# Performance work log

Hardware: AMD Instinct MI355X
Metric: run time of the kernel (lower is better)

Reference implementation:

```python
import jax, jax.numpy as jnp
import numpy as np

N = 100000
IN_C = 128
OUT_C = 200
E = 1600000


def gcn_conv(x, edge_index, W, b):
    """PyG GCNConv: symmetric degree-normalized aggregation with self-loops.
    out[v] = sum_{(u,v) in E+selfloops} d_u^-1/2 d_v^-1/2 (x_u @ W) + b
    """
    n = x.shape[0]
    xw = x @ W  # [N, out]
    loop = jnp.arange(n, dtype=edge_index.dtype)
    row = jnp.concatenate([edge_index[0], loop])  # src
    col = jnp.concatenate([edge_index[1], loop])  # dst
    ones = jnp.ones(row.shape[0], dtype=x.dtype)
    deg = jax.ops.segment_sum(ones, col, num_segments=n)  # in-degree incl. self
    dinv = jnp.where(deg > 0, jax.lax.rsqrt(deg), 0.0)
    norm = dinv[row] * dinv[col]  # [E+N]
    msgs = xw[row] * norm[:, None]  # [E+N, out]
    out = jax.ops.segment_sum(msgs, col, num_segments=n)
    return out + b


def setup_inputs() -> dict:
    key = jax.random.key(0)
    k1, k2, k3, k4 = jax.random.split(key, 4)
    x = jax.random.normal(k1, (N, IN_C), dtype=jnp.float32)
    edge_index = jax.random.randint(k2, (2, E), 0, N, dtype=jnp.int64)
    s1 = 1.0 / np.sqrt(IN_C)
    W1 = jax.random.uniform(k3, (IN_C, OUT_C), dtype=jnp.float32, minval=-s1, maxval=s1)
    b1 = jnp.zeros((OUT_C,), dtype=jnp.float32)
    W2 = jax.random.uniform(k4, (IN_C, OUT_C), dtype=jnp.float32, minval=-s1, maxval=s1)
    b2 = jnp.zeros((OUT_C,), dtype=jnp.float32)
    return {"x": x, "edge_index": edge_index, "W1": W1, "b1": b1, "W2": W2, "b2": b2}


def reference(x, edge_index, W1, b1, W2, b2):
    mu = gcn_conv(x, edge_index, W1, b1)
    logstd = gcn_conv(x, edge_index, W2, b2)
    return (mu, logstd)
```

## Files before the change

### kernel.cpp

```cpp
#include <hip/hip_runtime.h>

#define N_NODES 100000
#define IN_C    128
#define OUT_C   200
#define NT_TILES 13
#define KT_TILES 4

#define PSHIFT  8
#define NPB     256
#define NB      391
#define NB_POW2 512
#define BCAP    5120
#define PART_CH 4096
#define SEQ_P   16
#define SEQ_B   20

typedef __bf16 bf16_t;
typedef bf16_t bf16x8 __attribute__((ext_vector_type(8)));
typedef float  f32x4  __attribute__((ext_vector_type(4)));

__device__ __forceinline__ unsigned int bf16_bits(float f) {
    unsigned int u = __builtin_bit_cast(unsigned int, f);
    return (u + 0x7FFFu + ((u >> 16) & 1u)) >> 16;
}
__device__ __forceinline__ float bf16_lo(unsigned int p) {
    return __builtin_bit_cast(float, p << 16);
}
__device__ __forceinline__ float bf16_hi(unsigned int p) {
    return __builtin_bit_cast(float, p & 0xFFFF0000u);
}

__global__ __launch_bounds__(256) void partition_kernel(
        const int* __restrict__ row, const int* __restrict__ col, int E,
        int* __restrict__ gcount, unsigned int* __restrict__ gbuf) {
    __shared__ int hist[NB];
    __shared__ int base[NB];
    __shared__ int lofs[NB];
    __shared__ int pscan[256];
    __shared__ unsigned int stage[PART_CH];
    __shared__ unsigned short sb[PART_CH];
    const int tid = threadIdx.x;
    const int chunk = blockIdx.x * PART_CH;
    int cend = E - chunk; if (cend > PART_CH) cend = PART_CH;

    for (int i = tid; i < NB; i += 256) hist[i] = 0;
    __syncthreads();

    unsigned int   pay[SEQ_P];
    unsigned short eb[SEQ_P];
    unsigned short sq[SEQ_P];
    #pragma unroll
    for (int k = 0; k < SEQ_P; k++) {
        int i = tid + k * 256;
        eb[k] = 0xFFFFu;
        if (i < cend) {
            int c = __builtin_nontemporal_load(col + chunk + i);
            int r = __builtin_nontemporal_load(row + chunk + i);
            int b = (c >> PSHIFT) & (NB_POW2 - 1);
            if (b >= NB) b = NB - 1;
            pay[k] = (unsigned int)((c & (NPB - 1)) | (r << PSHIFT));
            eb[k]  = (unsigned short)b;
            sq[k]  = (unsigned short)atomicAdd(&hist[b], 1);
        }
    }
    __syncthreads();

    for (int i = tid; i < NB; i += 256)
        base[i] = atomicAdd(&gcount[i], hist[i]);

    int v0 = (2 * tid     < NB) ? hist[2 * tid]     : 0;
    int v1 = (2 * tid + 1 < NB) ? hist[2 * tid + 1] : 0;
    int s = v0 + v1;
    pscan[tid] = s;
    __syncthreads();
    for (int off = 1; off < 256; off <<= 1) {
        int u = (tid >= off) ? pscan[tid - off] : 0;
        __syncthreads();
        pscan[tid] += u;
        __syncthreads();
    }
    int ep = pscan[tid] - s;
    if (2 * tid     < NB) lofs[2 * tid]     = ep;
    if (2 * tid + 1 < NB) lofs[2 * tid + 1] = ep + v0;
    __syncthreads();

    #pragma unroll
    for (int k = 0; k < SEQ_P; k++) {
        if (eb[k] != 0xFFFFu) {
            int p = lofs[eb[k]] + sq[k];
            stage[p] = pay[k];
            sb[p] = eb[k];
        }
    }
    __syncthreads();

    for (int i = tid; i < cend; i += 256) {
        int b = sb[i];
        int p = base[b] + (i - lofs[b]);
        if (p < BCAP) gbuf[(size_t)b * BCAP + p] = stage[i];
    }
}

__global__ __launch_bounds__(256) void build_kernel(
        const unsigned int* __restrict__ gbuf, const int* __restrict__ gcount,
        const float* __restrict__ x,
        int* __restrict__ deg, int* __restrict__ offsets, float* __restrict__ dinv,
        int* __restrict__ csr_src, uint2* __restrict__ xs4, int n) {
    __shared__ int cnt[NPB];
    __shared__ int cur[NPB];
    __shared__ int pscan[256];
    __shared__ int gb[512];
    const int b = blockIdx.x;
    const int tid = threadIdx.x;

    int g0 = (2 * tid     < NB) ? gcount[2 * tid]     : 0;
    int g1 = (2 * tid + 1 < NB) ? gcount[2 * tid + 1] : 0;
    if (g0 > BCAP) g0 = BCAP;
    if (g1 > BCAP) g1 = BCAP;
    int gs = g0 + g1;
    pscan[tid] = gs;
    cnt[tid] = 0;
    __syncthreads();
    for (int off = 1; off < 256; off <<= 1) {
        int u = (tid >= off) ? pscan[tid - off] : 0;
        __syncthreads();
        pscan[tid] += u;
        __syncthreads();
    }
    int gep = pscan[tid] - gs;
    gb[2 * tid]     = gep;
    gb[2 * tid + 1] = gep + g0;
    __syncthreads();

    const int cbase = gb[b];
    int total = gcount[b]; if (total > BCAP) total = BCAP;
    const unsigned int* bp = gbuf + (size_t)b * BCAP;

    unsigned int   ee[SEQ_B];
    unsigned short sq[SEQ_B];
    #pragma unroll
    for (int k = 0; k < SEQ_B; k++) {
        int i = tid + k * 256;
        ee[k] = 0xFFFFFFFFu;
        if (i < total) {
            unsigned int e = __builtin_nontemporal_load(bp + i);
            ee[k] = e;
            sq[k] = (unsigned short)atomicAdd(&cnt[e & (NPB - 1)], 1);
        }
    }
    __syncthreads();

    int c = cnt[tid];
    pscan[tid] = c;
    __syncthreads();
    for (int off = 1; off < 256; off <<= 1) {
        int u = (tid >= off) ? pscan[tid - off] : 0;
        __syncthreads();
        pscan[tid] += u;
        __syncthreads();
    }
    int excl = pscan[tid] - c;
    cur[tid] = excl;
    int v = b * NPB + tid;
    if (v < n) {
        deg[v] = c;
        offsets[v] = cbase + excl;
        dinv[v] = rsqrtf((float)(c + 1));
    }
    __syncthreads();

    #pragma unroll
    for (int k = 0; k < SEQ_B; k++) {
        if (ee[k] != 0xFFFFFFFFu) {
            int p = cur[ee[k] & (NPB - 1)] + (int)sq[k];
            csr_src[cbase + p] = (int)(ee[k] >> PSHIFT);
        }
    }

    int wv = tid >> 6, ln = tid & 63;
    int hlf = ln >> 5, hl2 = ln & 31;
    for (int m = 0; m < 64; m += 2) {
        int local = wv * 64 + m + hlf;
        int nv = b * NPB + local;
        if (nv < n) {
            float dv = rsqrtf((float)(cnt[local] + 1));
            f32x4 f = __builtin_nontemporal_load((const f32x4*)x + (size_t)nv * 32 + hl2);
            uint2 o;
            o.x = bf16_bits(f.x * dv) | (bf16_bits(f.y * dv) << 16);
            o.y = bf16_bits(f.z * dv) | (bf16_bits(f.w * dv) << 16);
            xs4[(size_t)nv * 32 + hl2] = o;
        }
    }
}

__global__ __launch_bounds__(256) void gather_kernel(
        const uint2* __restrict__ xs4, const float* __restrict__ dinv,
        const int* __restrict__ offsets, const int* __restrict__ deg,
        const int* __restrict__ csr_src, uint2* __restrict__ agg4, int n) {
    int wave = threadIdx.x >> 6;
    int lane = threadIdx.x & 63;
    int half = lane >> 5;
    int hl   = lane & 31;
    int v = blockIdx.x * 4 + wave;
    if (v >= n) return;
    float dv = dinv[v];
    int start = offsets[v];
    int cnt = deg[v];
    float ax = 0.f, ay = 0.f, az = 0.f, aw = 0.f;

    const int* cp = csr_src + start;
    int i = 0;
    for (; i + 16 <= cnt; i += 16) {
        int u[8];
        #pragma unroll
        for (int j = 0; j < 8; j++) u[j] = __builtin_nontemporal_load(cp + i + 2 * j + half);
        uint2 t[8];
        #pragma unroll
        for (int j = 0; j < 8; j++) t[j] = xs4[(size_t)u[j] * 32 + hl];
        #pragma unroll
        for (int j = 0; j < 8; j++) {
            ax += bf16_lo(t[j].x); ay += bf16_hi(t[j].x);
            az += bf16_lo(t[j].y); aw += bf16_hi(t[j].y);
        }
    }
    if (i + 8 <= cnt) {
        int u[4];
        #pragma unroll
        for (int j = 0; j < 4; j++) u[j] = __builtin_nontemporal_load(cp + i + 2 * j + half);
        uint2 t[4];
        #pragma unroll
        for (int j = 0; j < 4; j++) t[j] = xs4[(size_t)u[j] * 32 + hl];
        #pragma unroll
        for (int j = 0; j < 4; j++) {
            ax += bf16_lo(t[j].x); ay += bf16_hi(t[j].x);
            az += bf16_lo(t[j].y); aw += bf16_hi(t[j].y);
        }
        i += 8;
    }
    if (i + 4 <= cnt) {
        int u[2];
        #pragma unroll
        for (int j = 0; j < 2; j++) u[j] = __builtin_nontemporal_load(cp + i + 2 * j + half);
        uint2 t[2];
        #pragma unroll
        for (int j = 0; j < 2; j++) t[j] = xs4[(size_t)u[j] * 32 + hl];
        #pragma unroll
        for (int j = 0; j < 2; j++) {
            ax += bf16_lo(t[j].x); ay += bf16_hi(t[j].x);
            az += bf16_lo(t[j].y); aw += bf16_hi(t[j].y);
        }
        i += 4;
    }
    if (i + 2 <= cnt) {
        int u = __builtin_nontemporal_load(cp + i + half);
        uint2 t = xs4[(size_t)u * 32 + hl];
        ax += bf16_lo(t.x); ay += bf16_hi(t.x);
        az += bf16_lo(t.y); aw += bf16_hi(t.y);
        i += 2;
    }
    if (i < cnt && half == 0) {
        int u = __builtin_nontemporal_load(cp + i);
        uint2 t = xs4[(size_t)u * 32 + hl];
        ax += bf16_lo(t.x); ay += bf16_hi(t.x);
        az += bf16_lo(t.y); aw += bf16_hi(t.y);
    }
    ax += __shfl_xor(ax, 32, 64);
    ay += __shfl_xor(ay, 32, 64);
    az += __shfl_xor(az, 32, 64);
    aw += __shfl_xor(aw, 32, 64);
    uint2 s = xs4[(size_t)v * 32 + hl];
    ax += bf16_lo(s.x); ay += bf16_hi(s.x);
    az += bf16_lo(s.y); aw += bf16_hi(s.y);
    if (half == 0) {
        uint2 o;
        o.x = bf16_bits(ax * dv) | (bf16_bits(ay * dv) << 16);
        o.y = bf16_bits(az * dv) | (bf16_bits(aw * dv) << 16);
        agg4[(size_t)v * 32 + hl] = o;
    }
}

__global__ void pack_w_kernel(const float* __restrict__ W1, const float* __restrict__ W2,
                              unsigned short* __restrict__ out) {
    int tid = blockIdx.x * blockDim.x + threadIdx.x;
    if (tid >= 2 * KT_TILES * NT_TILES * 64) return;
    int lane = tid & 63;
    int nt = (tid >> 6) % NT_TILES;
    int kt = (tid / (64 * NT_TILES)) % KT_TILES;
    int h  = tid / (64 * NT_TILES * KT_TILES);
    const float* W = h ? W2 : W1;
    int q = lane >> 4, r = lane & 15;
    int nn = nt * 16 + r;
    size_t dst = ((size_t)((nt * 2 + h) * KT_TILES + kt)) * 512 + (size_t)lane * 8;
    for (int j = 0; j < 8; j++) {
        int k = kt * 32 + q * 8 + j;
        float val = (nn < OUT_C) ? W[(size_t)k * OUT_C + nn] : 0.f;
        out[dst + j] = (unsigned short)bf16_bits(val);
    }
}

__global__ __launch_bounds__(256) void gemm_mfma_kernel(
        const unsigned short* __restrict__ agg,
        const unsigned short* __restrict__ Wpk,
        const float* __restrict__ b1, const float* __restrict__ b2,
        float* __restrict__ mu, float* __restrict__ ls, int M) {
    __shared__ uint4 Bs[2][512];
    int tid  = threadIdx.x;
    int wave = tid >> 6;
    int lane = tid & 63;
    int row0 = blockIdx.x * 64 + wave * 16;
    int q = lane >> 4, r = lane & 15;

    int arow = row0 + r; if (arow > M - 1) arow = M - 1;
    const unsigned short* ap = agg + (size_t)arow * IN_C + q * 8;
    bf16x8 afrag[KT_TILES];
    #pragma unroll
    for (int kt = 0; kt < KT_TILES; kt++) {
        uint4 u = *(const uint4*)(ap + kt * 32);
        afrag[kt] = __builtin_bit_cast(bf16x8, u);
    }

    f32x4 acc[2][NT_TILES];
    #pragma unroll
    for (int h = 0; h < 2; h++)
        #pragma unroll
        for (int nt = 0; nt < NT_TILES; nt++)
            acc[h][nt] = (f32x4){0.f, 0.f, 0.f, 0.f};

    const uint4* wsrc = (const uint4*)Wpk;
    uint4 pre0 = wsrc[tid];
    uint4 pre1 = wsrc[tid + 256];

    for (int nt = 0; nt < NT_TILES; nt++) {
        int buf = nt & 1;
        Bs[buf][tid]       = pre0;
        Bs[buf][tid + 256] = pre1;
        __syncthreads();
        if (nt + 1 < NT_TILES) {
            pre0 = wsrc[(nt + 1) * 512 + tid];
            pre1 = wsrc[(nt + 1) * 512 + tid + 256];
        }
        #pragma unroll
        for (int h = 0; h < 2; h++) {
            f32x4 c = acc[h][nt];
            #pragma unroll
            for (int kt = 0; kt < KT_TILES; kt++) {
                uint4 u = Bs[buf][(h * KT_TILES + kt) * 64 + lane];
                bf16x8 bfrag = __builtin_bit_cast(bf16x8, u);
                c = __builtin_amdgcn_mfma_f32_16x16x32_bf16(afrag[kt], bfrag, c, 0, 0, 0);
            }
            acc[h][nt] = c;
        }
    }

    float bv1r[NT_TILES], bv2r[NT_TILES];
    #pragma unroll
    for (int nt = 0; nt < NT_TILES; nt++) {
        int colx = nt * 16 + r;
        bool cok = colx < OUT_C;
        bv1r[nt] = cok ? b1[colx] : 0.f;
        bv2r[nt] = cok ? b2[colx] : 0.f;
    }
    #pragma unroll
    for (int reg = 0; reg < 4; reg++) {
        int gr = row0 + q * 4 + reg;
        if (gr < M) {
            float* mrow = mu + (size_t)gr * OUT_C;
            #pragma unroll
            for (int nt = 0; nt < NT_TILES; nt++) {
                int colx = nt * 16 + r;
                if (colx < OUT_C) mrow[colx] = acc[0][nt][reg] + bv1r[nt];
            }
            float* lrow = ls + (size_t)gr * OUT_C;
            #pragma unroll
            for (int nt = 0; nt < NT_TILES; nt++) {
                int colx = nt * 16 + r;
                if (colx < OUT_C) lrow[colx] = acc[1][nt][reg] + bv2r[nt];
            }
        }
    }
}

extern "C" void kernel_launch(void* const* d_in, const int* in_sizes, int n_in,
                              void* d_out, int out_size, void* d_ws, size_t ws_size,
                              hipStream_t stream) {
    const float* x  = (const float*)d_in[0];
    const int*   ei = (const int*)d_in[1];
    const float* W1 = (const float*)d_in[2];
    const float* b1 = (const float*)d_in[3];
    const float* W2 = (const float*)d_in[4];
    const float* b2 = (const float*)d_in[5];

    const int n = in_sizes[0] / IN_C;
    const int E = in_sizes[1] / 2;
    const int* row = ei;
    const int* col = ei + E;

    float* mu = (float*)d_out;
    float* ls = (float*)d_out + (size_t)n * OUT_C;

    char* ws = (char*)d_ws;
    int*            deg     = (int*)           (ws + 0);
    float*          dinv    = (float*)         (ws + 524288);
    int*            offsets = (int*)           (ws + 1048576);
    int*            gcount  = (int*)           (ws + 1572864);
    int*            csr_src = (int*)           (ws + 2162688);
    unsigned int*   xs2     = (unsigned int*)  (ws + 8562688);
    unsigned int*   gbuf    = (unsigned int*)  (ws + 34162688);
    unsigned int*   agg2    = (unsigned int*)  (ws + 42170368);
    unsigned short* Wpk     = (unsigned short*)(ws + 67770368);

    (void)hipMemsetAsync(gcount, 0, NB * sizeof(int), stream);

    pack_w_kernel<<<(2 * KT_TILES * NT_TILES * 64 + 255) / 256, 256, 0, stream>>>(W1, W2, Wpk);

    partition_kernel<<<(E + PART_CH - 1) / PART_CH, 256, 0, stream>>>(row, col, E, gcount, gbuf);

    build_kernel<<<NB, 256, 0, stream>>>(gbuf, gcount, x, deg, offsets, dinv,
                                         csr_src, (uint2*)xs2, n);

    gather_kernel<<<(n + 3) / 4, 256, 0, stream>>>(
        (const uint2*)xs2, dinv, offsets, deg, csr_src, (uint2*)agg2, n);

    gemm_mfma_kernel<<<(n + 63) / 64, 256, 0, stream>>>(
        (const unsigned short*)agg2, Wpk, b1, b2, mu, ls, n);
}
```

Baseline: 364.5 us.

## Widen gather to 16-byte loads with four edges per wave, pack offset/degree

The gather kernel now has each wave process four edges at once, with 16 lanes per edge each loading a 16-byte uint4 of bf16 features. The wave then reduces across the lane groups with two xor shuffles. Offset and degree are packed into a single int2 so one load fetches both. The gcount memset is folded into pack_w_kernel to drop one API call. This puts more gathers in flight per instruction at the cost of more accumulator registers and an extra shuffle stage, and the small remainder tail now runs with some lanes idle.

```diff
diff --git a/kernel.cpp b/kernel.cpp
--- a/kernel.cpp
+++ b/kernel.cpp
@@ -104,7 +104,7 @@
 __global__ __launch_bounds__(256) void build_kernel(
         const unsigned int* __restrict__ gbuf, const int* __restrict__ gcount,
         const float* __restrict__ x,
-        int* __restrict__ deg, int* __restrict__ offsets, float* __restrict__ dinv,
+        int2* __restrict__ od, float* __restrict__ dinv,
         int* __restrict__ csr_src, uint2* __restrict__ xs4, int n) {
     __shared__ int cnt[NPB];
     __shared__ int cur[NPB];
@@ -163,8 +163,7 @@
     cur[tid] = excl;
     int v = b * NPB + tid;
     if (v < n) {
-        deg[v] = c;
-        offsets[v] = cbase + excl;
+        od[v] = (int2){cbase + excl, c};
         dinv[v] = rsqrtf((float)(c + 1));
     }
     __syncthreads();
@@ -194,94 +193,86 @@
 }
 
 __global__ __launch_bounds__(256) void gather_kernel(
-        const uint2* __restrict__ xs4, const float* __restrict__ dinv,
-        const int* __restrict__ offsets, const int* __restrict__ deg,
-        const int* __restrict__ csr_src, uint2* __restrict__ agg4, int n) {
+        const uint4* __restrict__ xs16, const float* __restrict__ dinv,
+        const int2* __restrict__ od,
+        const int* __restrict__ csr_src, uint4* __restrict__ agg16, int n) {
     int wave = threadIdx.x >> 6;
     int lane = threadIdx.x & 63;
-    int half = lane >> 5;
-    int hl   = lane & 31;
+    int g = lane >> 4;
+    int w = lane & 15;
     int v = blockIdx.x * 4 + wave;
     if (v >= n) return;
     float dv = dinv[v];
-    int start = offsets[v];
-    int cnt = deg[v];
-    float ax = 0.f, ay = 0.f, az = 0.f, aw = 0.f;
+    int2 odv = od[v];
+    int start = odv.x, cnt = odv.y;
+    float a0 = 0.f, a1 = 0.f, a2 = 0.f, a3 = 0.f;
+    float a4 = 0.f, a5 = 0.f, a6 = 0.f, a7 = 0.f;
 
     const int* cp = csr_src + start;
     int i = 0;
     for (; i + 16 <= cnt; i += 16) {
-        int u[8];
+        int id4[4];
         #pragma unroll
-        for (int j = 0; j < 8; j++) u[j] = __builtin_nontemporal_load(cp + i + 2 * j + half);
-        uint2 t[8];
+        for (int j = 0; j < 4; j++)
+            id4[j] = __builtin_nontemporal_load(cp + i + 4 * j + g);
+        uint4 t[4];
         #pragma unroll
-        for (int j = 0; j < 8; j++) t[j] = xs4[(size_t)u[j] * 32 + hl];
-        #pragma unroll
-        for (int j = 0; j < 8; j++) {
-            ax += bf16_lo(t[j].x); ay += bf16_hi(t[j].x);
-            az += bf16_lo(t[j].y); aw += bf16_hi(t[j].y);
-        }
-    }
-    if (i + 8 <= cnt) {
-        int u[4];
-        #pragma unroll
-        for (int j = 0; j < 4; j++) u[j] = __builtin_nontemporal_load(cp + i + 2 * j + half);
-        uint2 t[4];
-        #pragma unroll
-        for (int j = 0; j < 4; j++) t[j] = xs4[(size_t)u[j] * 32 + hl];
+        for (int j = 0; j < 4; j++)
+            t[j] = xs16[(size_t)id4[j] * 16 + w];
         #pragma unroll
         for (int j = 0; j < 4; j++) {
-            ax += bf16_lo(t[j].x); ay += bf16_hi(t[j].x);
-            az += bf16_lo(t[j].y); aw += bf16_hi(t[j].y);
-        }
-        i += 8;
-    }
-    if (i + 4 <= cnt) {
-        int u[2];
-        #pragma unroll
-        for (int j = 0; j < 2; j++) u[j] = __builtin_nontemporal_load(cp + i + 2 * j + half);
-        uint2 t[2];
-        #pragma unroll
-        for (int j = 0; j < 2; j++) t[j] = xs4[(size_t)u[j] * 32 + hl];
-        #pragma unroll
-        for (int j = 0; j < 2; j++) {
-            ax += bf16_lo(t[j].x); ay += bf16_hi(t[j].x);
-            az += bf16_lo(t[j].y); aw += bf16_hi(t[j].y);
-        }
-        i += 4;
-    }
-    if (i + 2 <= cnt) {
-        int u = __builtin_nontemporal_load(cp + i + half);
-        uint2 t = xs4[(size_t)u * 32 + hl];
-        ax += bf16_lo(t.x); ay += bf16_hi(t.x);
-        az += bf16_lo(t.y); aw += bf16_hi(t.y);
-        i += 2;
-    }
-    if (i < cnt && half == 0) {
-        int u = __builtin_nontemporal_load(cp + i);
-        uint2 t = xs4[(size_t)u * 32 + hl];
-        ax += bf16_lo(t.x); ay += bf16_hi(t.x);
-        az += bf16_lo(t.y); aw += bf16_hi(t.y);
-    }
-    ax += __shfl_xor(ax, 32, 64);
-    ay += __shfl_xor(ay, 32, 64);
-    az += __shfl_xor(az, 32, 64);
-    aw += __shfl_xor(aw, 32, 64);
-    uint2 s = xs4[(size_t)v * 32 + hl];
-    ax += bf16_lo(s.x); ay += bf16_hi(s.x);
-    az += bf16_lo(s.y); aw += bf16_hi(s.y);
-    if (half == 0) {
-        uint2 o;
-        o.x = bf16_bits(ax * dv) | (bf16_bits(ay * dv) << 16);
-        o.y = bf16_bits(az * dv) | (bf16_bits(aw * dv) << 16);
-        agg4[(size_t)v * 32 + hl] = o;
+            a0 += bf16_lo(t[j].x); a1 += bf16_hi(t[j].x);
+            a2 += bf16_lo(t[j].y); a3 += bf16_hi(t[j].y);
+            a4 += bf16_lo(t[j].z); a5 += bf16_hi(t[j].z);
+            a6 += bf16_lo(t[j].w); a7 += bf16_hi(t[j].w);
+        }
+    }
+    for (; i + 4 <= cnt; i += 4) {
+        int idx = __builtin_nontemporal_load(cp + i + g);
+        uint4 t = xs16[(size_t)idx * 16 + w];
+        a0 += bf16_lo(t.x); a1 += bf16_hi(t.x);
+        a2 += bf16_lo(t.y); a3 += bf16_hi(t.y);
+        a4 += bf16_lo(t.z); a5 += bf16_hi(t.z);
+        a6 += bf16_lo(t.w); a7 += bf16_hi(t.w);
+    }
+    if (i < cnt) {
+        int e = i + g;
+        if (e < cnt) {
+            int idx = __builtin_nontemporal_load(cp + e);
+            uint4 t = xs16[(size_t)idx * 16 + w];
+            a0 += bf16_lo(t.x); a1 += bf16_hi(t.x);
+            a2 += bf16_lo(t.y); a3 += bf16_hi(t.y);
+            a4 += bf16_lo(t.z); a5 += bf16_hi(t.z);
+            a6 += bf16_lo(t.w); a7 += bf16_hi(t.w);
+        }
+    }
+    a0 += __shfl_xor(a0, 16, 64); a0 += __shfl_xor(a0, 32, 64);
+    a1 += __shfl_xor(a1, 16, 64); a1 += __shfl_xor(a1, 32, 64);
+    a2 += __shfl_xor(a2, 16, 64); a2 += __shfl_xor(a2, 32, 64);
+    a3 += __shfl_xor(a3, 16, 64); a3 += __shfl_xor(a3, 32, 64);
+    a4 += __shfl_xor(a4, 16, 64); a4 += __shfl_xor(a4, 32, 64);
+    a5 += __shfl_xor(a5, 16, 64); a5 += __shfl_xor(a5, 32, 64);
+    a6 += __shfl_xor(a6, 16, 64); a6 += __shfl_xor(a6, 32, 64);
+    a7 += __shfl_xor(a7, 16, 64); a7 += __shfl_xor(a7, 32, 64);
+    uint4 s = xs16[(size_t)v * 16 + w];
+    a0 += bf16_lo(s.x); a1 += bf16_hi(s.x);
+    a2 += bf16_lo(s.y); a3 += bf16_hi(s.y);
+    a4 += bf16_lo(s.z); a5 += bf16_hi(s.z);
+    a6 += bf16_lo(s.w); a7 += bf16_hi(s.w);
+    if (g == 0) {
+        uint4 o;
+        o.x = bf16_bits(a0 * dv) | (bf16_bits(a1 * dv) << 16);
+        o.y = bf16_bits(a2 * dv) | (bf16_bits(a3 * dv) << 16);
+        o.z = bf16_bits(a4 * dv) | (bf16_bits(a5 * dv) << 16);
+        o.w = bf16_bits(a6 * dv) | (bf16_bits(a7 * dv) << 16);
+        agg16[(size_t)v * 16 + w] = o;
     }
 }
 
 __global__ void pack_w_kernel(const float* __restrict__ W1, const float* __restrict__ W2,
-                              unsigned short* __restrict__ out) {
+                              unsigned short* __restrict__ out, int* __restrict__ gcount) {
     int tid = blockIdx.x * blockDim.x + threadIdx.x;
+    if (tid < NB) gcount[tid] = 0;
     if (tid >= 2 * KT_TILES * NT_TILES * 64) return;
     int lane = tid & 63;
     int nt = (tid >> 6) % NT_TILES;
@@ -399,9 +390,8 @@
     float* ls = (float*)d_out + (size_t)n * OUT_C;
 
     char* ws = (char*)d_ws;
-    int*            deg     = (int*)           (ws + 0);
-    float*          dinv    = (float*)         (ws + 524288);
-    int*            offsets = (int*)           (ws + 1048576);
+    int2*           od      = (int2*)          (ws + 0);
+    float*          dinv    = (float*)         (ws + 1048576);
     int*            gcount  = (int*)           (ws + 1572864);
     int*            csr_src = (int*)           (ws + 2162688);
     unsigned int*   xs2     = (unsigned int*)  (ws + 8562688);
@@ -409,17 +399,16 @@
     unsigned int*   agg2    = (unsigned int*)  (ws + 42170368);
     unsigned short* Wpk     = (unsigned short*)(ws + 67770368);
 
-    (void)hipMemsetAsync(gcount, 0, NB * sizeof(int), stream);
-
-    pack_w_kernel<<<(2 * KT_TILES * NT_TILES * 64 + 255) / 256, 256, 0, stream>>>(W1, W2, Wpk);
+    pack_w_kernel<<<(2 * KT_TILES * NT_TILES * 64 + 255) / 256, 256, 0, stream>>>(
+        W1, W2, Wpk, gcount);
 
     partition_kernel<<<(E + PART_CH - 1) / PART_CH, 256, 0, stream>>>(row, col, E, gcount, gbuf);
 
-    build_kernel<<<NB, 256, 0, stream>>>(gbuf, gcount, x, deg, offsets, dinv,
+    build_kernel<<<NB, 256, 0, stream>>>(gbuf, gcount, x, od, dinv,
                                          csr_src, (uint2*)xs2, n);
 
     gather_kernel<<<(n + 3) / 4, 256, 0, stream>>>(
-        (const uint2*)xs2, dinv, offsets, deg, csr_src, (uint2*)agg2, n);
+        (const uint4*)xs2, dinv, od, csr_src, (uint4*)agg2, n);
 
     gemm_mfma_kernel<<<(n + 63) / 64, 256, 0, stream>>>(
         (const unsigned short*)agg2, Wpk, b1, b2, mu, ls, n);
```

Result: no change. 360.9 us (-1.0%).
